# Optimization experiments

Measured on AMD Instinct MI355X. Metric: run time of the kernel, lower is better.

Reference implementation:

```python
import jax, jax.numpy as jnp
import numpy as np

B, Q, K, M, E, H = 2, 1024, 2048, 1024, 1024, 32
HD = E // H
SCALE = HD ** -0.5


def setup_inputs() -> dict:
    key0 = jax.random.key(0)
    ks = jax.random.split(key0, 12)
    inp = {
        "query": jax.random.normal(ks[0], (B, Q, E), jnp.float32),
        "key": jax.random.normal(ks[1], (B, K, E), jnp.float32),
        "value": jax.random.normal(ks[2], (B, K, E), jnp.float32),
        "memory": jax.random.normal(ks[3], (B, M, E), jnp.float32),
        "Wq": jax.random.normal(ks[4], (E, E), jnp.float32) * 0.02,
        "bq": jnp.zeros((E,), jnp.float32),
        "Wk": jax.random.normal(ks[5], (E, E), jnp.float32) * 0.02,
        "bk": jnp.zeros((E,), jnp.float32),
        "Wv": jax.random.normal(ks[6], (E, E), jnp.float32) * 0.02,
        "bv": jnp.zeros((E,), jnp.float32),
        "Wo": jax.random.normal(ks[7], (E, E), jnp.float32) * 0.02,
        "bo": jnp.zeros((E,), jnp.float32),
    }
    return inp


def _heads(x, W, b):
    # nn.Linear: y = x @ W.T + b, then split into heads -> (B, H, L, HD)
    y = jnp.einsum("ble,fe->blf", x, W) + b
    Bv, L, _ = y.shape
    return y.reshape(Bv, L, H, HD).transpose(0, 2, 1, 3)


def reference(query, key, value, memory, Wq, bq, Wk, bk, Wv, bv, Wo, bo):
    q = _heads(query, Wq, bq)        # (B,H,Q,HD)
    k = _heads(key, Wk, bk)          # (B,H,K,HD)
    v = _heads(value, Wv, bv)        # (B,H,K,HD)
    mk = _heads(memory, Wk, bk)      # (B,H,M,HD)
    mv = _heads(memory, Wv, bv)      # (B,H,M,HD)

    attn_scores = jnp.einsum("bhqd,bhkd->bhqk", q, k) * SCALE
    mem_scores = jnp.einsum("bhqd,bhmd->bhqm", q, mk) * SCALE
    combined = jnp.concatenate([attn_scores, mem_scores], axis=-1)  # (B,H,Q,K+M)
    w = jax.nn.softmax(combined, axis=-1)
    cv = jnp.concatenate([v, mv], axis=2)  # (B,H,K+M,HD)
    out = jnp.einsum("bhqk,bhkd->bhqd", w, cv)
    out = out.transpose(0, 2, 1, 3).reshape(query.shape[0], query.shape[1], E)
    return jnp.einsum("bqe,fe->bqf", out, Wo) + bo
```

## Files before the change

### kernel.cpp

```cpp
#include <hip/hip_runtime.h>


typedef float  f32x4  __attribute__((ext_vector_type(4)));
typedef short  bf16x8 __attribute__((ext_vector_type(8)));
typedef unsigned int   u32;
typedef unsigned short u16;
typedef u32 u32x2 __attribute__((ext_vector_type(2)));
typedef u32 u32x4 __attribute__((ext_vector_type(4)));
typedef u16 u16x4 __attribute__((ext_vector_type(4)));

#define SCALE_  0.17677669529663687f
#define LOG2E_  1.4426950408889634f

#if defined(__has_builtin)
#  if __has_builtin(__builtin_amdgcn_exp2f)
#    define EXP2F(x) __builtin_amdgcn_exp2f(x)
#  endif
#endif
#ifndef EXP2F
#  define EXP2F(x) __builtin_exp2f(x)
#endif

static __device__ __forceinline__ u32 bfpack2(float lo, float hi) {
  u32 a = __builtin_bit_cast(u32, lo) + 0x8000u;
  u32 b = __builtin_bit_cast(u32, hi) + 0x8000u;
  return __builtin_amdgcn_perm(b, a, 0x07060302u);
}
static __device__ __forceinline__ u16 bf16of(float x) {
  return (u16)((__builtin_bit_cast(u32, x) + 0x8000u) >> 16);
}
static __device__ __forceinline__ void gld_lds16(const u16* g, u16* l) {
  __builtin_amdgcn_global_load_lds(
      (const __attribute__((address_space(1))) void*)g,
      (__attribute__((address_space(3))) void*)l, 16, 0, 0);
}

__global__ __launch_bounds__(256)
void prep_kernel(const float* __restrict__ q, const float* __restrict__ k,
                 const float* __restrict__ v, const float* __restrict__ m,
                 const float* __restrict__ wq, const float* __restrict__ wk,
                 const float* __restrict__ wv, const float* __restrict__ wo,
                 u16* qs, u16* ks, u16* vs, u16* ms,
                 u16* wqs, u16* wks, u16* wvs, u16* wos) {
  const int bid = blockIdx.x;
  const float* src; u16* dst; int R, r0;
  if (bid < 32)       { src = q;  dst = qs;  R = 2048; r0 = bid * 64; }
  else if (bid < 96)  { src = k;  dst = ks;  R = 4096; r0 = (bid - 32) * 64; }
  else if (bid < 160) { src = v;  dst = vs;  R = 4096; r0 = (bid - 96) * 64; }
  else if (bid < 192) { src = m;  dst = ms;  R = 2048; r0 = (bid - 160) * 64; }
  else if (bid < 208) { src = wq; dst = wqs; R = 1024; r0 = (bid - 192) * 64; }
  else if (bid < 224) { src = wk; dst = wks; R = 1024; r0 = (bid - 208) * 64; }
  else if (bid < 240) { src = wv; dst = wvs; R = 1024; r0 = (bid - 224) * 64; }
  else                { src = wo; dst = wos; R = 1024; r0 = (bid - 240) * 64; }

  for (int i = 0; i < 32; ++i) {
    const int idx = i * 256 + threadIdx.x;
    const int kt  = idx >> 9;
    const int rem = idx & 511;
    const int row = rem >> 3;
    const int c   = rem & 7;
    const float* s = src + (size_t)(r0 + row) * 1024 + kt * 64 + c * 8;
    f32x4 a = *(const f32x4*)s, b = *(const f32x4*)(s + 4);
    u32x4 p;
    p.x = bfpack2(a.x, a.y); p.y = bfpack2(a.z, a.w);
    p.z = bfpack2(b.x, b.y); p.w = bfpack2(b.z, b.w);
    *(u32x4*)&dst[((size_t)kt * R + r0 + row) * 64 + ((c ^ (row & 7)) << 3)] = p;
  }
}

template <int MT, int OUT_BF16>
static __device__ __forceinline__
void gemm_tile(const u16* __restrict__ Abase, size_t row0, int RA,
               const u16* __restrict__ Wsw, const float* __restrict__ bias,
               void* __restrict__ Cout, float scale,
               int bm, int bn, u16* As, u16* Bs) {
  constexpr int MI = MT / 32;
  const int tid  = threadIdx.x;
  const int lane = tid & 63;
  const int wave = tid >> 6;
  const int ln   = lane & 15;
  const int quad = lane >> 4;
  const int wm   = wave >> 1;
  const int wn   = wave & 1;

  f32x4 acc[MI][4];
#pragma unroll
  for (int i = 0; i < MI; ++i)
#pragma unroll
    for (int j = 0; j < 4; ++j)
      acc[i][j] = (f32x4){0.f, 0.f, 0.f, 0.f};

  for (int kt = 0; kt < 16; ++kt) {
    const u16* Ag = Abase + ((size_t)kt * RA + row0) * 64;
    const u16* Bg = Wsw + ((size_t)kt * 1024 + bn * 128) * 64;
#pragma unroll
    for (int r = 0; r < MI; ++r) {
      const int ii = wave * MI + r;
      gld_lds16(Ag + ii * 512 + lane * 8, &As[ii * 512]);
    }
#pragma unroll
    for (int r = 0; r < 4; ++r) {
      const int ii = wave * 4 + r;
      gld_lds16(Bg + ii * 512 + lane * 8, &Bs[ii * 512]);
    }
    __syncthreads();

#pragma unroll
    for (int kk = 0; kk < 2; ++kk) {
      bf16x8 af[MI], bfr[4];
#pragma unroll
      for (int mi = 0; mi < MI; ++mi) {
        const int row = wm * (MI * 16) + mi * 16 + ln;
        af[mi] = *(const bf16x8*)&As[row * 64 + (((kk * 4 + quad) ^ (ln & 7)) << 3)];
      }
#pragma unroll
      for (int ni = 0; ni < 4; ++ni) {
        const int row = wn * 64 + ni * 16 + ln;
        bfr[ni] = *(const bf16x8*)&Bs[row * 64 + (((kk * 4 + quad) ^ (ln & 7)) << 3)];
      }
#pragma unroll
      for (int mi = 0; mi < MI; ++mi)
#pragma unroll
        for (int ni = 0; ni < 4; ++ni)
          acc[mi][ni] = __builtin_amdgcn_mfma_f32_16x16x32_bf16(af[mi], bfr[ni], acc[mi][ni], 0, 0, 0);
    }
    __syncthreads();
  }

#pragma unroll
  for (int ni = 0; ni < 4; ++ni) {
    const int gc = bn * 128 + wn * 64 + ni * 16 + ln;
    const float bval = bias[gc];
#pragma unroll
    for (int mi = 0; mi < MI; ++mi) {
      const int gr = bm * MT + wm * (MI * 16) + mi * 16 + quad * 4;
#pragma unroll
      for (int r = 0; r < 4; ++r) {
        const float vv = (acc[mi][ni][r] + bval) * scale;
        if (OUT_BF16)
          ((u16*)Cout)[(size_t)(gr + r) * 1024 + gc] = bf16of(vv);
        else
          ((float*)Cout)[(size_t)(gr + r) * 1024 + gc] = vv;
      }
    }
  }
}

__global__ __launch_bounds__(256)
void proj3_kernel(const u16* __restrict__ query_sw,
                  const u16* __restrict__ key_sw,
                  const u16* __restrict__ value_sw,
                  const u16* __restrict__ mem_sw,
                  const u16* __restrict__ Wq_sw, const float* __restrict__ bq,
                  const u16* __restrict__ Wk_sw, const float* __restrict__ bk,
                  const u16* __restrict__ Wv_sw, const float* __restrict__ bv,
                  u16* qp, u16* kcat, u16* vcat) {
  __shared__ u16 As[128 * 64];
  __shared__ u16 Bs[128 * 64];
  const int bx = blockIdx.x, bn = blockIdx.y;

  const u16* Abase; size_t row0; int RA, bm;
  const u16* W; const float* bias; u16* C; float scale;

  if (bx < 16) {
    bm = bx; Abase = query_sw; row0 = (size_t)bm * 128; RA = 2048;
    W = Wq_sw; bias = bq; C = qp; scale = SCALE_ * LOG2E_;
  } else {
    const int bxx = (bx < 64) ? (bx - 16) : (bx - 64);
    bm = bxx;
    const int gr0 = bxx * 128;
    const int bb  = gr0 / 3072;
    const int i0  = gr0 - bb * 3072;
    const u16* seq = (bx < 64) ? key_sw : value_sw;
    if (i0 < 2048) { Abase = seq;    row0 = (size_t)bb * 2048 + i0;        RA = 4096; }
    else           { Abase = mem_sw; row0 = (size_t)bb * 1024 + (i0 - 2048); RA = 2048; }
    if (bx < 64) { W = Wk_sw; bias = bk; C = kcat; }
    else         { W = Wv_sw; bias = bv; C = vcat; }
    scale = 1.0f;
  }
  gemm_tile<128, 1>(Abase, row0, RA, W, bias, C, scale, bm, bn, As, Bs);
}

__global__ __launch_bounds__(256)
void gemm_out_kernel(const u16* __restrict__ attn_sw,
                     const u16* __restrict__ Wo_sw,
                     const float* __restrict__ bo,
                     float* __restrict__ out) {
  __shared__ u16 As[64 * 64];
  __shared__ u16 Bs[128 * 64];
  gemm_tile<64, 0>(attn_sw, (size_t)blockIdx.x * 64, 2048, Wo_sw, bo,
                   (void*)out, 1.0f, blockIdx.x, blockIdx.y, As, Bs);
}

__global__ __launch_bounds__(256)
void transpose_v_kernel(const u16* __restrict__ vcat, u16* __restrict__ vT) {
  __shared__ u16 T[32][132];
  const int tid = threadIdx.x;
  const int l0  = blockIdx.x * 128;
  const int bh  = blockIdx.y;
  const int b   = bh >> 5, h = bh & 31;

#pragma unroll
  for (int j = 0; j < 4; ++j) {
    const int c = tid + 256 * j;
    const int row  = c >> 3;
    const int col4 = (c & 7) * 4;
    u16x4 v = *(const u16x4*)&vcat[(size_t)(b * 3072 + l0 + row) * 1024 + h * 32 + col4];
    T[col4 + 0][row] = v.x; T[col4 + 1][row] = v.y;
    T[col4 + 2][row] = v.z; T[col4 + 3][row] = v.w;
  }
  __syncthreads();
#pragma unroll
  for (int j = 0; j < 4; ++j) {
    const int c = tid + 256 * j;
    const int d   = c >> 5;
    const int rem = c & 31;
    const int ch  = rem >> 4;
    const int x   = rem & 15;
    u16x4 v;
    v.x = T[d][ch * 64 + x +  0];
    v.y = T[d][ch * 64 + x + 16];
    v.z = T[d][ch * 64 + x + 32];
    v.w = T[d][ch * 64 + x + 48];
    *(u16x4*)&vT[(size_t)(bh * 32 + d) * 3072 + l0 + ch * 64 + x * 4] = v;
  }
}

__global__ __launch_bounds__(256, 6)
void attn_kernel(const u16* __restrict__ qp,
                 const u16* __restrict__ kcat,
                 const u16* __restrict__ vTp,
                 u16* __restrict__ attn_sw) {
  __shared__ u16 PwAll[4 * 32 * 72];

  const int tid  = threadIdx.x;
  const int lane = tid & 63;
  const int wave = tid >> 6;
  const int ln   = lane & 15;
  const int quad = lane >> 4;
  const int bid  = blockIdx.x;
  const int bh   = bid & 63;
  const int qt   = bid >> 6;
  const int b    = bh >> 5;
  const int h    = bh & 31;
  const int q0   = qt * 32;

  bf16x8 qf[2];
#pragma unroll
  for (int mf = 0; mf < 2; ++mf)
    qf[mf] = *(const bf16x8*)&qp[(size_t)(b * 1024 + q0 + mf * 16 + ln) * 1024 + h * 32 + quad * 8];

  f32x4 acc[2][2], accS[2];
#pragma unroll
  for (int mf = 0; mf < 2; ++mf) {
    accS[mf] = (f32x4){0.f, 0.f, 0.f, 0.f};
#pragma unroll
    for (int df = 0; df < 2; ++df) acc[mf][df] = (f32x4){0.f, 0.f, 0.f, 0.f};
  }
  bf16x8 ones;
#pragma unroll
  for (int i = 0; i < 8; ++i) ones[i] = (short)0x3F80;

  const u16* kbase = kcat + (size_t)(b * 3072) * 1024 + h * 32;
  const u16* vbase = vTp + (size_t)(bh * 32) * 3072;
  u16* Pw = &PwAll[wave * (32 * 72)];

  const u16* kp[4];
  const u16* vp[2];
#pragma unroll
  for (int nf = 0; nf < 4; ++nf)
    kp[nf] = kbase + (size_t)(wave * 768 + nf * 16 + ln) * 1024 + quad * 8;
#pragma unroll
  for (int df = 0; df < 2; ++df)
    vp[df] = vbase + (size_t)(df * 16 + ln) * 3072 + wave * 768 + quad * 8;

  for (int ci = 0; ci < 12; ++ci) {
    bf16x8 kf[4], vf[4];
#pragma unroll
    for (int nf = 0; nf < 4; ++nf)
      kf[nf] = *(const bf16x8*)kp[nf];
#pragma unroll
    for (int kk = 0; kk < 2; ++kk)
#pragma unroll
      for (int df = 0; df < 2; ++df)
        vf[kk * 2 + df] = *(const bf16x8*)(vp[df] + kk * 32);

    f32x4 s[2][4];
#pragma unroll
    for (int mf = 0; mf < 2; ++mf)
#pragma unroll
      for (int nf = 0; nf < 4; ++nf)
        s[mf][nf] = __builtin_amdgcn_mfma_f32_16x16x32_bf16(qf[mf], kf[nf],
                                                            (f32x4){0.f, 0.f, 0.f, 0.f}, 0, 0, 0);

#pragma unroll
    for (int mf = 0; mf < 2; ++mf)
#pragma unroll
      for (int r = 0; r < 4; ++r) {
        const float p0 = EXP2F(s[mf][0][r]);
        const float p1 = EXP2F(s[mf][1][r]);
        const float p2 = EXP2F(s[mf][2][r]);
        const float p3 = EXP2F(s[mf][3][r]);
        u32x2 pk;
        pk.x = bfpack2(p0, p1);
        pk.y = bfpack2(p2, p3);
        *(u32x2*)&Pw[(mf * 16 + quad * 4 + r) * 72 + ln * 4] = pk;
      }

#pragma unroll
    for (int kk = 0; kk < 2; ++kk)
#pragma unroll
      for (int mf = 0; mf < 2; ++mf) {
        bf16x8 pf = *(const bf16x8*)&Pw[(mf * 16 + ln) * 72 + kk * 32 + quad * 8];
        accS[mf] = __builtin_amdgcn_mfma_f32_16x16x32_bf16(pf, ones, accS[mf], 0, 0, 0);
#pragma unroll
        for (int df = 0; df < 2; ++df)
          acc[mf][df] = __builtin_amdgcn_mfma_f32_16x16x32_bf16(pf, vf[kk * 2 + df], acc[mf][df], 0, 0, 0);
      }

#pragma unroll
    for (int nf = 0; nf < 4; ++nf) kp[nf] += 64 * 1024;
#pragma unroll
    for (int df = 0; df < 2; ++df) vp[df] += 64;
  }

  __syncthreads();
  f32x4* CA = (f32x4*)PwAll;
  f32x4* CS = (f32x4*)&PwAll[8192];
#pragma unroll
  for (int mf = 0; mf < 2; ++mf) {
#pragma unroll
    for (int df = 0; df < 2; ++df)
      CA[((wave * 2 + mf) * 2 + df) * 64 + lane] = acc[mf][df];
    if (ln == 0) CS[(wave * 2 + mf) * 4 + quad] = accS[mf];
  }
  __syncthreads();

  if (wave == 0) {
    const int j = ln & 7, chi = ln >> 3;
#pragma unroll
    for (int mf = 0; mf < 2; ++mf) {
      f32x4 l = CS[(0 + mf) * 4 + quad];
#pragma unroll
      for (int w = 1; w < 4; ++w) l += CS[((w * 2) + mf) * 4 + quad];
      f32x4 inv;
#pragma unroll
      for (int r = 0; r < 4; ++r) inv[r] = 1.0f / l[r];
#pragma unroll
      for (int df = 0; df < 2; ++df) {
        f32x4 t = CA[((0 + mf) * 2 + df) * 64 + lane];
#pragma unroll
        for (int w = 1; w < 4; ++w) t += CA[(((w * 2) + mf) * 2 + df) * 64 + lane];
        const int c = (h & 1) * 4 + df * 2 + chi;
#pragma unroll
        for (int r = 0; r < 4; ++r) {
          const int row = b * 1024 + q0 + mf * 16 + quad * 4 + r;
          const int cp  = c ^ ((quad * 4 + r) & 7);
          attn_sw[((size_t)(h >> 1) * 2048 + row) * 64 + cp * 8 + j] = bf16of(t[r] * inv[r]);
        }
      }
    }
  }
}

extern "C" void kernel_launch(void* const* d_in, const int* in_sizes, int n_in,
                              void* d_out, int out_size, void* d_ws, size_t ws_size,
                              hipStream_t stream) {
  (void)in_sizes; (void)n_in; (void)out_size; (void)ws_size;
  const float* query  = (const float*)d_in[0];
  const float* key    = (const float*)d_in[1];
  const float* value  = (const float*)d_in[2];
  const float* memory = (const float*)d_in[3];
  const float* Wq = (const float*)d_in[4];
  const float* bq = (const float*)d_in[5];
  const float* Wk = (const float*)d_in[6];
  const float* bk = (const float*)d_in[7];
  const float* Wv = (const float*)d_in[8];
  const float* bv = (const float*)d_in[9];
  const float* Wo = (const float*)d_in[10];
  const float* bo = (const float*)d_in[11];
  float* out = (float*)d_out;

  char* ws = (char*)d_ws;
  const size_t MB = 1024 * 1024;
  u16* query_sw = (u16*)(ws + 0 * MB);
  u16* key_sw   = (u16*)(ws + 4 * MB);
  u16* value_sw = (u16*)(ws + 12 * MB);
  u16* mem_sw   = (u16*)(ws + 20 * MB);
  u16* Wq_sw    = (u16*)(ws + 24 * MB);
  u16* Wk_sw    = (u16*)(ws + 26 * MB);
  u16* Wv_sw    = (u16*)(ws + 28 * MB);
  u16* Wo_sw    = (u16*)(ws + 30 * MB);
  u16* qp       = (u16*)(ws + 32 * MB);
  u16* kcat     = (u16*)(ws + 36 * MB);
  u16* vcat     = (u16*)(ws + 48 * MB);
  u16* vT       = (u16*)(ws + 60 * MB);
  u16* attn_sw  = (u16*)(ws + 72 * MB);

  dim3 blk(256);
  prep_kernel<<<dim3(256), blk, 0, stream>>>(query, key, value, memory, Wq, Wk, Wv, Wo,
                                             query_sw, key_sw, value_sw, mem_sw,
                                             Wq_sw, Wk_sw, Wv_sw, Wo_sw);
  proj3_kernel<<<dim3(112, 8), blk, 0, stream>>>(query_sw, key_sw, value_sw, mem_sw,
                                                 Wq_sw, bq, Wk_sw, bk, Wv_sw, bv,
                                                 qp, kcat, vcat);
  transpose_v_kernel<<<dim3(24, 64), blk, 0, stream>>>(vcat, vT);
  attn_kernel<<<dim3(2048), blk, 0, stream>>>(qp, kcat, vT, attn_sw);
  gemm_out_kernel<<<dim3(32, 8), blk, 0, stream>>>(attn_sw, Wo_sw, bo, out);
}
```

Measured before the change: 282.9 us.

## Fuse V transpose into projection epilogue and double attention query tile

The V projection epilogue now transposes its tile through shared memory and writes the head-major transposed V layout directly. This removes the separate transpose kernel and the vcat round trip through global memory. The attention kernel now handles 64 query rows per block instead of 32, halving the grid and reusing each loaded K/V fragment across twice as many rows. All four waves now share the final reduction. In exchange the kernel uses more registers and LDS, and the occupancy hint drops from 6 to 3 blocks.

```diff
diff --git a/kernel.cpp b/kernel.cpp
--- a/kernel.cpp
+++ b/kernel.cpp
@@ -68,12 +68,11 @@
   }
 }
 
-template <int MT, int OUT_BF16>
+template <int MT>
 static __device__ __forceinline__
-void gemm_tile(const u16* __restrict__ Abase, size_t row0, int RA,
-               const u16* __restrict__ Wsw, const float* __restrict__ bias,
-               void* __restrict__ Cout, float scale,
-               int bm, int bn, u16* As, u16* Bs) {
+void gemm_core(const u16* __restrict__ Abase, size_t row0, int RA,
+               const u16* __restrict__ Wsw, int bn,
+               u16* As, u16* Bs, f32x4 acc[][4]) {
   constexpr int MI = MT / 32;
   const int tid  = threadIdx.x;
   const int lane = tid & 63;
@@ -83,7 +82,6 @@
   const int wm   = wave >> 1;
   const int wn   = wave & 1;
 
-  f32x4 acc[MI][4];
 #pragma unroll
   for (int i = 0; i < MI; ++i)
 #pragma unroll
@@ -125,24 +123,6 @@
           acc[mi][ni] = __builtin_amdgcn_mfma_f32_16x16x32_bf16(af[mi], bfr[ni], acc[mi][ni], 0, 0, 0);
     }
     __syncthreads();
-  }
-
-#pragma unroll
-  for (int ni = 0; ni < 4; ++ni) {
-    const int gc = bn * 128 + wn * 64 + ni * 16 + ln;
-    const float bval = bias[gc];
-#pragma unroll
-    for (int mi = 0; mi < MI; ++mi) {
-      const int gr = bm * MT + wm * (MI * 16) + mi * 16 + quad * 4;
-#pragma unroll
-      for (int r = 0; r < 4; ++r) {
-        const float vv = (acc[mi][ni][r] + bval) * scale;
-        if (OUT_BF16)
-          ((u16*)Cout)[(size_t)(gr + r) * 1024 + gc] = bf16of(vv);
-        else
-          ((float*)Cout)[(size_t)(gr + r) * 1024 + gc] = vv;
-      }
-    }
   }
 }
 
@@ -154,31 +134,87 @@
                   const u16* __restrict__ Wq_sw, const float* __restrict__ bq,
                   const u16* __restrict__ Wk_sw, const float* __restrict__ bk,
                   const u16* __restrict__ Wv_sw, const float* __restrict__ bv,
-                  u16* qp, u16* kcat, u16* vcat) {
-  __shared__ u16 As[128 * 64];
-  __shared__ u16 Bs[128 * 64];
+                  u16* qp, u16* kcat, u16* vT) {
+  __shared__ u16 SH[16896];
+  u16* As = SH;
+  u16* Bs = SH + 8192;
+
+  const int tid  = threadIdx.x;
+  const int lane = tid & 63;
+  const int wave = tid >> 6;
+  const int ln   = lane & 15;
+  const int quad = lane >> 4;
+  const int wm   = wave >> 1;
+  const int wn   = wave & 1;
   const int bx = blockIdx.x, bn = blockIdx.y;
 
-  const u16* Abase; size_t row0; int RA, bm;
-  const u16* W; const float* bias; u16* C; float scale;
+  const u16* Abase; size_t row0; int RA, bm, bb, l0;
+  const u16* W; const float* bias;
 
   if (bx < 16) {
     bm = bx; Abase = query_sw; row0 = (size_t)bm * 128; RA = 2048;
-    W = Wq_sw; bias = bq; C = qp; scale = SCALE_ * LOG2E_;
+    W = Wq_sw; bias = bq; bb = 0; l0 = 0;
   } else {
     const int bxx = (bx < 64) ? (bx - 16) : (bx - 64);
     bm = bxx;
     const int gr0 = bxx * 128;
-    const int bb  = gr0 / 3072;
-    const int i0  = gr0 - bb * 3072;
+    bb = gr0 / 3072;
+    l0 = gr0 - bb * 3072;
     const u16* seq = (bx < 64) ? key_sw : value_sw;
-    if (i0 < 2048) { Abase = seq;    row0 = (size_t)bb * 2048 + i0;        RA = 4096; }
-    else           { Abase = mem_sw; row0 = (size_t)bb * 1024 + (i0 - 2048); RA = 2048; }
-    if (bx < 64) { W = Wk_sw; bias = bk; C = kcat; }
-    else         { W = Wv_sw; bias = bv; C = vcat; }
-    scale = 1.0f;
-  }
-  gemm_tile<128, 1>(Abase, row0, RA, W, bias, C, scale, bm, bn, As, Bs);
+    if (l0 < 2048) { Abase = seq;    row0 = (size_t)bb * 2048 + l0;          RA = 4096; }
+    else           { Abase = mem_sw; row0 = (size_t)bb * 1024 + (l0 - 2048); RA = 2048; }
+    if (bx < 64) { W = Wk_sw; bias = bk; }
+    else         { W = Wv_sw; bias = bv; }
+  }
+
+  f32x4 acc[4][4];
+  gemm_core<128>(Abase, row0, RA, W, bn, As, Bs, acc);
+
+  if (bx < 64) {
+    u16* C = (bx < 16) ? qp : kcat;
+    const float scale = (bx < 16) ? (SCALE_ * LOG2E_) : 1.0f;
+#pragma unroll
+    for (int ni = 0; ni < 4; ++ni) {
+      const int gc = bn * 128 + wn * 64 + ni * 16 + ln;
+      const float bval = bias[gc];
+#pragma unroll
+      for (int mi = 0; mi < 4; ++mi) {
+        const int gr = bm * 128 + wm * 64 + mi * 16 + quad * 4;
+#pragma unroll
+        for (int r = 0; r < 4; ++r)
+          C[(size_t)(gr + r) * 1024 + gc] = bf16of((acc[mi][ni][r] + bval) * scale);
+      }
+    }
+  } else {
+    u16* T = SH;
+#pragma unroll
+    for (int ni = 0; ni < 4; ++ni) {
+      const int fl = wn * 64 + ni * 16 + ln;
+      const float bval = bias[bn * 128 + fl];
+#pragma unroll
+      for (int mi = 0; mi < 4; ++mi) {
+        const int kl = wm * 64 + mi * 16 + quad * 4;
+#pragma unroll
+        for (int r = 0; r < 4; ++r)
+          T[(kl + r) * 132 + fl] = bf16of(acc[mi][ni][r] + bval);
+      }
+    }
+    __syncthreads();
+    const int fr = tid >> 1;
+    const int ch = tid & 1;
+    const int fg = bn * 128 + fr;
+    const size_t rowg = ((size_t)bb * 32 + (fg >> 5)) * 32 + (fg & 31);
+    u16* dstrow = vT + rowg * 3072 + l0 + ch * 64;
+#pragma unroll
+    for (int x = 0; x < 16; ++x) {
+      u16x4 v;
+      v.x = T[(ch * 64 + x +  0) * 132 + fr];
+      v.y = T[(ch * 64 + x + 16) * 132 + fr];
+      v.z = T[(ch * 64 + x + 32) * 132 + fr];
+      v.w = T[(ch * 64 + x + 48) * 132 + fr];
+      *(u16x4*)&dstrow[x * 4] = v;
+    }
+  }
 }
 
 __global__ __launch_bounds__(256)
@@ -188,50 +224,38 @@
                      float* __restrict__ out) {
   __shared__ u16 As[64 * 64];
   __shared__ u16 Bs[128 * 64];
-  gemm_tile<64, 0>(attn_sw, (size_t)blockIdx.x * 64, 2048, Wo_sw, bo,
-                   (void*)out, 1.0f, blockIdx.x, blockIdx.y, As, Bs);
-}
-
-__global__ __launch_bounds__(256)
-void transpose_v_kernel(const u16* __restrict__ vcat, u16* __restrict__ vT) {
-  __shared__ u16 T[32][132];
-  const int tid = threadIdx.x;
-  const int l0  = blockIdx.x * 128;
-  const int bh  = blockIdx.y;
-  const int b   = bh >> 5, h = bh & 31;
-
-#pragma unroll
-  for (int j = 0; j < 4; ++j) {
-    const int c = tid + 256 * j;
-    const int row  = c >> 3;
-    const int col4 = (c & 7) * 4;
-    u16x4 v = *(const u16x4*)&vcat[(size_t)(b * 3072 + l0 + row) * 1024 + h * 32 + col4];
-    T[col4 + 0][row] = v.x; T[col4 + 1][row] = v.y;
-    T[col4 + 2][row] = v.z; T[col4 + 3][row] = v.w;
-  }
-  __syncthreads();
-#pragma unroll
-  for (int j = 0; j < 4; ++j) {
-    const int c = tid + 256 * j;
-    const int d   = c >> 5;
-    const int rem = c & 31;
-    const int ch  = rem >> 4;
-    const int x   = rem & 15;
-    u16x4 v;
-    v.x = T[d][ch * 64 + x +  0];
-    v.y = T[d][ch * 64 + x + 16];
-    v.z = T[d][ch * 64 + x + 32];
-    v.w = T[d][ch * 64 + x + 48];
-    *(u16x4*)&vT[(size_t)(bh * 32 + d) * 3072 + l0 + ch * 64 + x * 4] = v;
-  }
-}
-
-__global__ __launch_bounds__(256, 6)
+  const int tid  = threadIdx.x;
+  const int lane = tid & 63;
+  const int wave = tid >> 6;
+  const int ln   = lane & 15;
+  const int quad = lane >> 4;
+  const int wm   = wave >> 1;
+  const int wn   = wave & 1;
+  const int bm = blockIdx.x, bn = blockIdx.y;
+
+  f32x4 acc[2][4];
+  gemm_core<64>(attn_sw, (size_t)bm * 64, 2048, Wo_sw, bn, As, Bs, acc);
+
+#pragma unroll
+  for (int ni = 0; ni < 4; ++ni) {
+    const int gc = bn * 128 + wn * 64 + ni * 16 + ln;
+    const float bval = bo[gc];
+#pragma unroll
+    for (int mi = 0; mi < 2; ++mi) {
+      const int gr = bm * 64 + wm * 32 + mi * 16 + quad * 4;
+#pragma unroll
+      for (int r = 0; r < 4; ++r)
+        out[(size_t)(gr + r) * 1024 + gc] = acc[mi][ni][r] + bval;
+    }
+  }
+}
+
+__global__ __launch_bounds__(256, 3)
 void attn_kernel(const u16* __restrict__ qp,
                  const u16* __restrict__ kcat,
                  const u16* __restrict__ vTp,
                  u16* __restrict__ attn_sw) {
-  __shared__ u16 PwAll[4 * 32 * 72];
+  __shared__ u16 PwAll[4 * 64 * 72];
 
   const int tid  = threadIdx.x;
   const int lane = tid & 63;
@@ -243,16 +267,16 @@
   const int qt   = bid >> 6;
   const int b    = bh >> 5;
   const int h    = bh & 31;
-  const int q0   = qt * 32;
-
-  bf16x8 qf[2];
-#pragma unroll
-  for (int mf = 0; mf < 2; ++mf)
+  const int q0   = qt * 64;
+
+  bf16x8 qf[4];
+#pragma unroll
+  for (int mf = 0; mf < 4; ++mf)
     qf[mf] = *(const bf16x8*)&qp[(size_t)(b * 1024 + q0 + mf * 16 + ln) * 1024 + h * 32 + quad * 8];
 
-  f32x4 acc[2][2], accS[2];
-#pragma unroll
-  for (int mf = 0; mf < 2; ++mf) {
+  f32x4 acc[4][2], accS[4];
+#pragma unroll
+  for (int mf = 0; mf < 4; ++mf) {
     accS[mf] = (f32x4){0.f, 0.f, 0.f, 0.f};
 #pragma unroll
     for (int df = 0; df < 2; ++df) acc[mf][df] = (f32x4){0.f, 0.f, 0.f, 0.f};
@@ -263,7 +287,7 @@
 
   const u16* kbase = kcat + (size_t)(b * 3072) * 1024 + h * 32;
   const u16* vbase = vTp + (size_t)(bh * 32) * 3072;
-  u16* Pw = &PwAll[wave * (32 * 72)];
+  u16* Pw = &PwAll[wave * (64 * 72)];
 
   const u16* kp[4];
   const u16* vp[2];
@@ -285,32 +309,30 @@
       for (int df = 0; df < 2; ++df)
         vf[kk * 2 + df] = *(const bf16x8*)(vp[df] + kk * 32);
 
-    f32x4 s[2][4];
-#pragma unroll
-    for (int mf = 0; mf < 2; ++mf)
+#pragma unroll
+    for (int mf = 0; mf < 4; ++mf) {
+      f32x4 s[4];
 #pragma unroll
       for (int nf = 0; nf < 4; ++nf)
-        s[mf][nf] = __builtin_amdgcn_mfma_f32_16x16x32_bf16(qf[mf], kf[nf],
-                                                            (f32x4){0.f, 0.f, 0.f, 0.f}, 0, 0, 0);
-
-#pragma unroll
-    for (int mf = 0; mf < 2; ++mf)
+        s[nf] = __builtin_amdgcn_mfma_f32_16x16x32_bf16(qf[mf], kf[nf],
+                                                        (f32x4){0.f, 0.f, 0.f, 0.f}, 0, 0, 0);
 #pragma unroll
       for (int r = 0; r < 4; ++r) {
-        const float p0 = EXP2F(s[mf][0][r]);
-        const float p1 = EXP2F(s[mf][1][r]);
-        const float p2 = EXP2F(s[mf][2][r]);
-        const float p3 = EXP2F(s[mf][3][r]);
+        const float p0 = EXP2F(s[0][r]);
+        const float p1 = EXP2F(s[1][r]);
+        const float p2 = EXP2F(s[2][r]);
+        const float p3 = EXP2F(s[3][r]);
         u32x2 pk;
         pk.x = bfpack2(p0, p1);
         pk.y = bfpack2(p2, p3);
         *(u32x2*)&Pw[(mf * 16 + quad * 4 + r) * 72 + ln * 4] = pk;
       }
+    }
 
 #pragma unroll
     for (int kk = 0; kk < 2; ++kk)
 #pragma unroll
-      for (int mf = 0; mf < 2; ++mf) {
+      for (int mf = 0; mf < 4; ++mf) {
         bf16x8 pf = *(const bf16x8*)&Pw[(mf * 16 + ln) * 72 + kk * 32 + quad * 8];
         accS[mf] = __builtin_amdgcn_mfma_f32_16x16x32_bf16(pf, ones, accS[mf], 0, 0, 0);
 #pragma unroll
@@ -326,38 +348,36 @@
 
   __syncthreads();
   f32x4* CA = (f32x4*)PwAll;
-  f32x4* CS = (f32x4*)&PwAll[8192];
-#pragma unroll
-  for (int mf = 0; mf < 2; ++mf) {
+  f32x4* CS = (f32x4*)&PwAll[16384];
+#pragma unroll
+  for (int mf = 0; mf < 4; ++mf) {
 #pragma unroll
     for (int df = 0; df < 2; ++df)
-      CA[((wave * 2 + mf) * 2 + df) * 64 + lane] = acc[mf][df];
-    if (ln == 0) CS[(wave * 2 + mf) * 4 + quad] = accS[mf];
+      CA[((wave * 4 + mf) * 2 + df) * 64 + lane] = acc[mf][df];
+    if (ln == 0) CS[(wave * 4 + mf) * 4 + quad] = accS[mf];
   }
   __syncthreads();
 
-  if (wave == 0) {
+  {
+    const int mf = wave;
     const int j = ln & 7, chi = ln >> 3;
-#pragma unroll
-    for (int mf = 0; mf < 2; ++mf) {
-      f32x4 l = CS[(0 + mf) * 4 + quad];
-#pragma unroll
-      for (int w = 1; w < 4; ++w) l += CS[((w * 2) + mf) * 4 + quad];
-      f32x4 inv;
-#pragma unroll
-      for (int r = 0; r < 4; ++r) inv[r] = 1.0f / l[r];
-#pragma unroll
-      for (int df = 0; df < 2; ++df) {
-        f32x4 t = CA[((0 + mf) * 2 + df) * 64 + lane];
-#pragma unroll
-        for (int w = 1; w < 4; ++w) t += CA[(((w * 2) + mf) * 2 + df) * 64 + lane];
-        const int c = (h & 1) * 4 + df * 2 + chi;
-#pragma unroll
-        for (int r = 0; r < 4; ++r) {
-          const int row = b * 1024 + q0 + mf * 16 + quad * 4 + r;
-          const int cp  = c ^ ((quad * 4 + r) & 7);
-          attn_sw[((size_t)(h >> 1) * 2048 + row) * 64 + cp * 8 + j] = bf16of(t[r] * inv[r]);
-        }
+    f32x4 l = CS[mf * 4 + quad];
+#pragma unroll
+    for (int w = 1; w < 4; ++w) l += CS[((w * 4) + mf) * 4 + quad];
+    f32x4 inv;
+#pragma unroll
+    for (int r = 0; r < 4; ++r) inv[r] = 1.0f / l[r];
+#pragma unroll
+    for (int df = 0; df < 2; ++df) {
+      f32x4 t = CA[(mf * 2 + df) * 64 + lane];
+#pragma unroll
+      for (int w = 1; w < 4; ++w) t += CA[(((w * 4) + mf) * 2 + df) * 64 + lane];
+      const int c = (h & 1) * 4 + df * 2 + chi;
+#pragma unroll
+      for (int r = 0; r < 4; ++r) {
+        const int row = b * 1024 + q0 + mf * 16 + quad * 4 + r;
+        const int cp  = c ^ ((quad * 4 + r) & 7);
+        attn_sw[((size_t)(h >> 1) * 2048 + row) * 64 + cp * 8 + j] = bf16of(t[r] * inv[r]);
       }
     }
   }
@@ -393,9 +413,8 @@
   u16* Wo_sw    = (u16*)(ws + 30 * MB);
   u16* qp       = (u16*)(ws + 32 * MB);
   u16* kcat     = (u16*)(ws + 36 * MB);
-  u16* vcat     = (u16*)(ws + 48 * MB);
-  u16* vT       = (u16*)(ws + 60 * MB);
-  u16* attn_sw  = (u16*)(ws + 72 * MB);
+  u16* vT       = (u16*)(ws + 48 * MB);
+  u16* attn_sw  = (u16*)(ws + 60 * MB);
 
   dim3 blk(256);
   prep_kernel<<<dim3(256), blk, 0, stream>>>(query, key, value, memory, Wq, Wk, Wv, Wo,
@@ -403,8 +422,7 @@
                                              Wq_sw, Wk_sw, Wv_sw, Wo_sw);
   proj3_kernel<<<dim3(112, 8), blk, 0, stream>>>(query_sw, key_sw, value_sw, mem_sw,
                                                  Wq_sw, bq, Wk_sw, bk, Wv_sw, bv,
-                                                 qp, kcat, vcat);
-  transpose_v_kernel<<<dim3(24, 64), blk, 0, stream>>>(vcat, vT);
-  attn_kernel<<<dim3(2048), blk, 0, stream>>>(qp, kcat, vT, attn_sw);
+                                                 qp, kcat, vT);
+  attn_kernel<<<dim3(1024), blk, 0, stream>>>(qp, kcat, vT, attn_sw);
   gemm_out_kernel<<<dim3(32, 8), blk, 0, stream>>>(attn_sw, Wo_sw, bo, out);
 }
```

Result: faster. 235.5 us (-16.8%).
